# Kernel optimization log

Hardware: AMD Instinct MI355X
Metric: run time of the kernel (lower is better)

Reference implementation:

```python
import jax, jax.numpy as jnp
import numpy as np

EPS = 1e-12  # torch F.normalize eps

def _l2norm(v, axis):
    return v / jnp.maximum(jnp.linalg.norm(v, axis=axis, keepdims=True), EPS)

def setup_inputs() -> dict:
    key = jax.random.key(0)
    k1, k2, k3, k4 = jax.random.split(key, 4)
    n, K, d, H, W = 32, 64, 256, 64, 64
    x = jax.random.normal(k1, (n, d, H, W), dtype=jnp.float32)
    conv_w = jax.random.normal(k2, (K, d), dtype=jnp.float32) * 0.05
    conv_b = jax.random.normal(k3, (K,), dtype=jnp.float32) * 0.05
    centroids = jax.random.uniform(k4, (K, d), dtype=jnp.float32)
    return {"x": x, "conv_w": conv_w, "conv_b": conv_b, "centroids": centroids}

def reference(x, conv_w, conv_b, centroids):
    n, c, H, W = x.shape
    K = centroids.shape[0]
    # input L2 normalization over channel dim
    x = _l2norm(x, axis=1)
    x_flat = x.reshape(n, c, H * W)                      # [n, c, S]
    # 1x1 conv == matmul over channels, then softmax over clusters
    logits = jnp.einsum('kc,ncs->nks', conv_w, x_flat) + conv_b[None, :, None]
    a = jax.nn.softmax(logits, axis=1)                   # [n, K, S]
    # vlad[n,k,c] = sum_s a[n,k,s] * (x[n,c,s] - cent[k,c])
    #            = (a @ x^T) - cent * sum_s a   (GEMM reformulation)
    vlad = jnp.einsum('nks,ncs->nkc', a, x_flat)
    vlad = vlad - a.sum(axis=2)[:, :, None] * centroids[None, :, :]
    # intra-normalize per cluster, flatten, global L2 normalize
    vlad = _l2norm(vlad, axis=2)
    vlad = vlad.reshape(n, K * c)
    vlad = _l2norm(vlad, axis=1)
    return vlad
```

## Files before the change

### kernel.cpp

```cpp
#include <hip/hip_runtime.h>
#include <math.h>

#define NIMG 32
#define CDIM 256
#define KCL  64
#define SPIX 4096

__global__ __launch_bounds__(256) void k_wt(const float* __restrict__ w, float* __restrict__ wT) {
    int g = blockIdx.x * 256 + threadIdx.x;
    if (g < KCL * CDIM) {
        int k = g / CDIM, c = g % CDIM;
        wT[c * KCL + k] = w[g];
    }
}

#define WFMA32() \
    acc[0]=fmaf(w0_.x,xv,acc[0]);   acc[1]=fmaf(w0_.y,xv,acc[1]); \
    acc[2]=fmaf(w0_.z,xv,acc[2]);   acc[3]=fmaf(w0_.w,xv,acc[3]); \
    acc[4]=fmaf(w1_.x,xv,acc[4]);   acc[5]=fmaf(w1_.y,xv,acc[5]); \
    acc[6]=fmaf(w1_.z,xv,acc[6]);   acc[7]=fmaf(w1_.w,xv,acc[7]); \
    acc[8]=fmaf(w2_.x,xv,acc[8]);   acc[9]=fmaf(w2_.y,xv,acc[9]); \
    acc[10]=fmaf(w2_.z,xv,acc[10]); acc[11]=fmaf(w2_.w,xv,acc[11]); \
    acc[12]=fmaf(w3_.x,xv,acc[12]); acc[13]=fmaf(w3_.y,xv,acc[13]); \
    acc[14]=fmaf(w3_.z,xv,acc[14]); acc[15]=fmaf(w3_.w,xv,acc[15]); \
    acc[16]=fmaf(w4_.x,xv,acc[16]); acc[17]=fmaf(w4_.y,xv,acc[17]); \
    acc[18]=fmaf(w4_.z,xv,acc[18]); acc[19]=fmaf(w4_.w,xv,acc[19]); \
    acc[20]=fmaf(w5_.x,xv,acc[20]); acc[21]=fmaf(w5_.y,xv,acc[21]); \
    acc[22]=fmaf(w5_.z,xv,acc[22]); acc[23]=fmaf(w5_.w,xv,acc[23]); \
    acc[24]=fmaf(w6_.x,xv,acc[24]); acc[25]=fmaf(w6_.y,xv,acc[25]); \
    acc[26]=fmaf(w6_.z,xv,acc[26]); acc[27]=fmaf(w6_.w,xv,acc[27]); \
    acc[28]=fmaf(w7_.x,xv,acc[28]); acc[29]=fmaf(w7_.y,xv,acc[29]); \
    acc[30]=fmaf(w7_.z,xv,acc[30]); acc[31]=fmaf(w7_.w,xv,acc[31]);

__global__ __launch_bounds__(512, 4) void k_logits(const float* __restrict__ x,
                                                   const float* __restrict__ wT,
                                                   const float* __restrict__ b,
                                                   float* __restrict__ aT,
                                                   float* __restrict__ inv_norm,
                                                   float* __restrict__ asum_part) {
    int blk = blockIdx.x;
    int n = blk >> 4, g = blk & 15;
    int s0 = g * 256;
    int tid = threadIdx.x;
    int wv = tid >> 6, l = tid & 63;
    int sl = tid & 255;
    int khu = __builtin_amdgcn_readfirstlane(tid >> 8);

    __shared__ float xs[32 * 256];
    __shared__ float4 red4[8 * 64];
    __shared__ float redf[512];
    __shared__ float invs[256];

    float acc[32];
    #pragma unroll
    for (int i = 0; i < 32; i++) acc[i] = 0.f;
    float4 sq = {0.f, 0.f, 0.f, 0.f};

    int cst = tid >> 6;
    int p4 = (tid & 63) * 4;

    for (int t = 0; t < 8; t++) {
        if (t) __syncthreads();
        #pragma unroll
        for (int i = 0; i < 4; i++) {
            int c = cst + 8 * i;
            float4 xq = *(const float4*)(x + ((size_t)(n * CDIM + t * 32 + c)) * SPIX + s0 + p4);
            sq.x = fmaf(xq.x, xq.x, sq.x);
            sq.y = fmaf(xq.y, xq.y, sq.y);
            sq.z = fmaf(xq.z, xq.z, sq.z);
            sq.w = fmaf(xq.w, xq.w, sq.w);
            *(float4*)(xs + c * 256 + p4) = xq;
        }
        __syncthreads();
        const float* wrow = wT + (size_t)(t * 32) * KCL + khu * 32;
        for (int cc = 0; cc < 32; cc++) {
            float xv = xs[cc * 256 + sl];
            const float4* wp = (const float4*)(wrow + (size_t)cc * KCL);
            float4 w0_=wp[0], w1_=wp[1], w2_=wp[2], w3_=wp[3];
            float4 w4_=wp[4], w5_=wp[5], w6_=wp[6], w7_=wp[7];
            WFMA32()
        }
    }

    red4[wv * 64 + l] = sq;
    __syncthreads();
    if (wv == 0) {
        float4 ssq = red4[l];
        #pragma unroll
        for (int i = 1; i < 8; i++) {
            float4 t4 = red4[i * 64 + l];
            ssq.x += t4.x; ssq.y += t4.y; ssq.z += t4.z; ssq.w += t4.w;
        }
        float4 invn;
        invn.x = 1.f / fmaxf(sqrtf(ssq.x), 1e-12f);
        invn.y = 1.f / fmaxf(sqrtf(ssq.y), 1e-12f);
        invn.z = 1.f / fmaxf(sqrtf(ssq.z), 1e-12f);
        invn.w = 1.f / fmaxf(sqrtf(ssq.w), 1e-12f);
        *(float4*)(invs + 4 * l) = invn;
        *(float4*)(inv_norm + (size_t)n * SPIX + s0 + 4 * l) = invn;
    }
    __syncthreads();
    float invp = invs[sl];

    const float* bb = b + khu * 32;
    #pragma unroll
    for (int i = 0; i < 32; i++) acc[i] = fmaf(acc[i], invp, bb[i]);

    float m = acc[0];
    #pragma unroll
    for (int i = 1; i < 32; i++) m = fmaxf(m, acc[i]);
    redf[tid] = m;
    __syncthreads();
    m = fmaxf(redf[sl], redf[256 + sl]);
    float ssum = 0.f;
    #pragma unroll
    for (int i = 0; i < 32; i++) { float e = __expf(acc[i] - m); acc[i] = e; ssum += e; }
    __syncthreads();
    redf[tid] = ssum;
    __syncthreads();
    float r = 1.0f / (redf[sl] + redf[256 + sl]);
    #pragma unroll
    for (int i = 0; i < 32; i++) acc[i] *= r;

    float4* ap = (float4*)(aT + ((size_t)(n * SPIX + s0 + sl)) * KCL + khu * 32);
    #pragma unroll
    for (int j = 0; j < 8; j++) {
        float4 v = {acc[4*j+0], acc[4*j+1], acc[4*j+2], acc[4*j+3]};
        ap[j] = v;
    }

    #pragma unroll
    for (int i = 0; i < 32; i++) {
        float v = acc[i];
        #pragma unroll
        for (int off = 32; off > 0; off >>= 1) v += __shfl_xor(v, off, 64);
        if (l == 0) asum_part[(blk * 8 + wv) * 32 + i] = v;
    }
}

__global__ __launch_bounds__(512, 4) void k_vlad(const float* __restrict__ x,
                                                 const float* __restrict__ inv_norm,
                                                 const float* __restrict__ aT,
                                                 float* __restrict__ vlad_part) {
    int blk = blockIdx.x;
    int n = blk >> 4, g = blk & 15;
    int tid = threadIdx.x;
    int kh = __builtin_amdgcn_readfirstlane(tid >> 8);
    int c = tid & 255;

    __shared__ float xt[256 * 33];

    float acc[32];
    #pragma unroll
    for (int i = 0; i < 32; i++) acc[i] = 0.f;

    int sl = tid & 31;
    int cr = tid >> 5;

    for (int t = 0; t < 8; t++) {
        int s0 = g * 256 + t * 32;
        float invp = inv_norm[n * SPIX + s0 + sl];
        __syncthreads();
        #pragma unroll
        for (int i = 0; i < 16; i++) {
            int cc = cr + i * 16;
            xt[cc * 33 + sl] = x[((size_t)n * CDIM + cc) * SPIX + s0 + sl] * invp;
        }
        __syncthreads();

        const float* ab = aT + ((size_t)(n * SPIX + s0)) * KCL + kh * 32;
        for (int ss = 0; ss < 32; ss++) {
            float xn = xt[c * 33 + ss];
            const float4* ap = (const float4*)(ab + ss * 64);
            #pragma unroll
            for (int q = 0; q < 8; q++) {
                float4 a4 = ap[q];
                acc[4*q+0] = fmaf(a4.x, xn, acc[4*q+0]);
                acc[4*q+1] = fmaf(a4.y, xn, acc[4*q+1]);
                acc[4*q+2] = fmaf(a4.z, xn, acc[4*q+2]);
                acc[4*q+3] = fmaf(a4.w, xn, acc[4*q+3]);
            }
        }
    }
    float* vp = vlad_part + ((size_t)blk * KCL + kh * 32) * CDIM + c;
    #pragma unroll
    for (int i = 0; i < 32; i++) vp[(size_t)i * CDIM] = acc[i];
}

__global__ __launch_bounds__(256) void k_combine(const float* __restrict__ vlad_part,
                                                 const float* __restrict__ asum_part,
                                                 const float* __restrict__ cent,
                                                 float* __restrict__ out,
                                                 float* __restrict__ rs) {
    int blk = blockIdx.x;
    int n = blk >> 6, k = blk & 63;
    int c = threadIdx.x;
    float v = 0.f;
    for (int j = 0; j < 16; j++)
        v += vlad_part[(((size_t)(n * 16 + j)) * KCL + k) * CDIM + c];
    float as = 0.f;
    int kh = k >> 5, kj = k & 31;
    for (int j = 0; j < 16; j++)
        for (int q = 0; q < 4; q++)
            as += asum_part[(((n * 16 + j) * 8) + kh * 4 + q) * 32 + kj];
    v = fmaf(-as, cent[k * CDIM + c], v);

    float t = v * v;
    #pragma unroll
    for (int off = 32; off > 0; off >>= 1) t += __shfl_xor(t, off, 64);
    __shared__ float w4[4];
    int lane = threadIdx.x & 63, wid = threadIdx.x >> 6;
    if (lane == 0) w4[wid] = t;
    __syncthreads();
    float ss = w4[0] + w4[1] + w4[2] + w4[3];
    float inv = 1.0f / fmaxf(sqrtf(ss), 1e-12f);
    out[(size_t)blk * CDIM + c] = v * inv;
    if (threadIdx.x == 0) rs[blk] = ss * inv * inv;
}

__global__ __launch_bounds__(256) void k_gnorm(const float* __restrict__ rs,
                                               float* __restrict__ out) {
    int n = blockIdx.x >> 3, j = blockIdx.x & 7;
    float ss = 0.f;
    for (int k = 0; k < KCL; k++) ss += rs[n * KCL + k];
    float g = 1.0f / fmaxf(sqrtf(ss), 1e-12f);
    size_t base = (size_t)n * (KCL * CDIM) + j * 2048 + threadIdx.x;
    for (int i = 0; i < 8; i++) out[base + i * 256] *= g;
}

extern "C" void kernel_launch(void* const* d_in, const int* in_sizes, int n_in,
                              void* d_out, int out_size, void* d_ws, size_t ws_size,
                              hipStream_t stream) {
    const float* x    = (const float*)d_in[0];
    const float* w    = (const float*)d_in[1];
    const float* b    = (const float*)d_in[2];
    const float* cent = (const float*)d_in[3];
    float* out = (float*)d_out;

    float* ws = (float*)d_ws;
    float* wT        = ws;
    float* inv_norm  = wT + 16384;
    float* aT        = inv_norm + 131072;
    float* vlad_part = aT + 8388608;
    float* asum_part = vlad_part + 8388608;
    float* rs        = asum_part + 131072;

    k_wt<<<64, 256, 0, stream>>>(w, wT);
    k_logits<<<512, 512, 0, stream>>>(x, wT, b, aT, inv_norm, asum_part);
    k_vlad<<<512, 512, 0, stream>>>(x, inv_norm, aT, vlad_part);
    k_combine<<<2048, 256, 0, stream>>>(vlad_part, asum_part, cent, out, rs);
    k_gnorm<<<256, 256, 0, stream>>>(rs, out);
}
```

Before: 184.8 us.

## Double-buffer x tiles via direct global-to-LDS loads and compute norms from LDS

Replaces the register-staged load of each 32-channel x tile with async global_load_lds into a double-buffered shared array, so the next tile is prefetched while the current one is consumed by the FMA loop. The per-pixel squared norm is now accumulated from the LDS values inside the compute loop, which removes the separate cross-wave reduction and its extra shared buffers and barriers. The cost is twice the xs shared memory (64KB), which may reduce occupancy under the 512x4 launch bounds, plus an extra barrier per iteration. It also relies on manual vmcnt waits being correct.

```diff
diff --git a/kernel.cpp b/kernel.cpp
--- a/kernel.cpp
+++ b/kernel.cpp
@@ -45,62 +45,54 @@
     int wv = tid >> 6, l = tid & 63;
     int sl = tid & 255;
     int khu = __builtin_amdgcn_readfirstlane(tid >> 8);
-
-    __shared__ float xs[32 * 256];
-    __shared__ float4 red4[8 * 64];
+    int wvu = __builtin_amdgcn_readfirstlane(wv);
+
+    __shared__ float xs[2][32 * 256];
     __shared__ float redf[512];
-    __shared__ float invs[256];
 
     float acc[32];
     #pragma unroll
     for (int i = 0; i < 32; i++) acc[i] = 0.f;
-    float4 sq = {0.f, 0.f, 0.f, 0.f};
-
-    int cst = tid >> 6;
-    int p4 = (tid & 63) * 4;
+    float nrm = 0.f;
+
+    #define STAGE(T, BUF) { \
+        _Pragma("unroll") \
+        for (int i_ = 0; i_ < 4; i_++) { \
+            int row_ = wvu + 8 * i_; \
+            const float* src_ = x + ((size_t)(n * CDIM + (T) * 32 + row_)) * SPIX + s0 + 4 * l; \
+            float* dst_ = &xs[BUF][row_ * 256] + 4 * l; \
+            __builtin_amdgcn_global_load_lds( \
+                (const __attribute__((address_space(1))) unsigned int*)src_, \
+                (__attribute__((address_space(3))) unsigned int*)dst_, 16, 0, 0); \
+        } }
+
+    STAGE(0, 0)
 
     for (int t = 0; t < 8; t++) {
-        if (t) __syncthreads();
-        #pragma unroll
-        for (int i = 0; i < 4; i++) {
-            int c = cst + 8 * i;
-            float4 xq = *(const float4*)(x + ((size_t)(n * CDIM + t * 32 + c)) * SPIX + s0 + p4);
-            sq.x = fmaf(xq.x, xq.x, sq.x);
-            sq.y = fmaf(xq.y, xq.y, sq.y);
-            sq.z = fmaf(xq.z, xq.z, sq.z);
-            sq.w = fmaf(xq.w, xq.w, sq.w);
-            *(float4*)(xs + c * 256 + p4) = xq;
-        }
-        __syncthreads();
+        int buf = t & 1;
+        if (t < 7) {
+            STAGE(t + 1, buf ^ 1)
+            asm volatile("s_waitcnt vmcnt(4)" ::: "memory");
+        } else {
+            asm volatile("s_waitcnt vmcnt(0)" ::: "memory");
+        }
+        __syncthreads();
+
         const float* wrow = wT + (size_t)(t * 32) * KCL + khu * 32;
+        const float* xrow = xs[buf];
         for (int cc = 0; cc < 32; cc++) {
-            float xv = xs[cc * 256 + sl];
+            float xv = xrow[cc * 256 + sl];
+            nrm = fmaf(xv, xv, nrm);
             const float4* wp = (const float4*)(wrow + (size_t)cc * KCL);
             float4 w0_=wp[0], w1_=wp[1], w2_=wp[2], w3_=wp[3];
             float4 w4_=wp[4], w5_=wp[5], w6_=wp[6], w7_=wp[7];
             WFMA32()
         }
-    }
-
-    red4[wv * 64 + l] = sq;
-    __syncthreads();
-    if (wv == 0) {
-        float4 ssq = red4[l];
-        #pragma unroll
-        for (int i = 1; i < 8; i++) {
-            float4 t4 = red4[i * 64 + l];
-            ssq.x += t4.x; ssq.y += t4.y; ssq.z += t4.z; ssq.w += t4.w;
-        }
-        float4 invn;
-        invn.x = 1.f / fmaxf(sqrtf(ssq.x), 1e-12f);
-        invn.y = 1.f / fmaxf(sqrtf(ssq.y), 1e-12f);
-        invn.z = 1.f / fmaxf(sqrtf(ssq.z), 1e-12f);
-        invn.w = 1.f / fmaxf(sqrtf(ssq.w), 1e-12f);
-        *(float4*)(invs + 4 * l) = invn;
-        *(float4*)(inv_norm + (size_t)n * SPIX + s0 + 4 * l) = invn;
-    }
-    __syncthreads();
-    float invp = invs[sl];
+        __syncthreads();
+    }
+
+    float invp = 1.f / fmaxf(sqrtf(nrm), 1e-12f);
+    if (khu == 0) inv_norm[(size_t)n * SPIX + s0 + sl] = invp;
 
     const float* bb = b + khu * 32;
     #pragma unroll
```

New measurement: 208.8 us. +13.0%, slower.

## Store soft-assignments in k-quad planar layout and move cluster sums to separate kernel

Applied to the files above, without the earlier changes.

The assignment matrix is now written in a planar layout grouped by four clusters per plane, instead of [pixel][64] rows. This lets the k_vlad loads and a new k_asum reduction kernel read contiguous float4 streams. The per-pixel squared norm is now computed from the shared-memory tile inside the channel loop, which removes the cross-wave reduction and two barriers. The shuffle-based asum reduction leaves k_logits and becomes an extra kernel launch that rereads the whole assignment buffer (about 32MB). In k_vlad the 8 float4 loads per pixel now hit 8 separate planes instead of one contiguous 128-byte row.

```diff
diff --git a/kernel.cpp b/kernel.cpp
--- a/kernel.cpp
+++ b/kernel.cpp
@@ -36,25 +36,21 @@
                                                    const float* __restrict__ wT,
                                                    const float* __restrict__ b,
                                                    float* __restrict__ aT,
-                                                   float* __restrict__ inv_norm,
-                                                   float* __restrict__ asum_part) {
+                                                   float* __restrict__ inv_norm) {
     int blk = blockIdx.x;
     int n = blk >> 4, g = blk & 15;
     int s0 = g * 256;
     int tid = threadIdx.x;
-    int wv = tid >> 6, l = tid & 63;
     int sl = tid & 255;
     int khu = __builtin_amdgcn_readfirstlane(tid >> 8);
 
     __shared__ float xs[32 * 256];
-    __shared__ float4 red4[8 * 64];
     __shared__ float redf[512];
-    __shared__ float invs[256];
 
     float acc[32];
     #pragma unroll
     for (int i = 0; i < 32; i++) acc[i] = 0.f;
-    float4 sq = {0.f, 0.f, 0.f, 0.f};
+    float nrm = 0.f;
 
     int cst = tid >> 6;
     int p4 = (tid & 63) * 4;
@@ -65,16 +61,13 @@
         for (int i = 0; i < 4; i++) {
             int c = cst + 8 * i;
             float4 xq = *(const float4*)(x + ((size_t)(n * CDIM + t * 32 + c)) * SPIX + s0 + p4);
-            sq.x = fmaf(xq.x, xq.x, sq.x);
-            sq.y = fmaf(xq.y, xq.y, sq.y);
-            sq.z = fmaf(xq.z, xq.z, sq.z);
-            sq.w = fmaf(xq.w, xq.w, sq.w);
             *(float4*)(xs + c * 256 + p4) = xq;
         }
         __syncthreads();
         const float* wrow = wT + (size_t)(t * 32) * KCL + khu * 32;
         for (int cc = 0; cc < 32; cc++) {
             float xv = xs[cc * 256 + sl];
+            nrm = fmaf(xv, xv, nrm);
             const float4* wp = (const float4*)(wrow + (size_t)cc * KCL);
             float4 w0_=wp[0], w1_=wp[1], w2_=wp[2], w3_=wp[3];
             float4 w4_=wp[4], w5_=wp[5], w6_=wp[6], w7_=wp[7];
@@ -82,25 +75,8 @@
         }
     }
 
-    red4[wv * 64 + l] = sq;
-    __syncthreads();
-    if (wv == 0) {
-        float4 ssq = red4[l];
-        #pragma unroll
-        for (int i = 1; i < 8; i++) {
-            float4 t4 = red4[i * 64 + l];
-            ssq.x += t4.x; ssq.y += t4.y; ssq.z += t4.z; ssq.w += t4.w;
-        }
-        float4 invn;
-        invn.x = 1.f / fmaxf(sqrtf(ssq.x), 1e-12f);
-        invn.y = 1.f / fmaxf(sqrtf(ssq.y), 1e-12f);
-        invn.z = 1.f / fmaxf(sqrtf(ssq.z), 1e-12f);
-        invn.w = 1.f / fmaxf(sqrtf(ssq.w), 1e-12f);
-        *(float4*)(invs + 4 * l) = invn;
-        *(float4*)(inv_norm + (size_t)n * SPIX + s0 + 4 * l) = invn;
-    }
-    __syncthreads();
-    float invp = invs[sl];
+    float invp = 1.f / fmaxf(sqrtf(nrm), 1e-12f);
+    if (khu == 0) inv_norm[(size_t)n * SPIX + s0 + sl] = invp;
 
     const float* bb = b + khu * 32;
     #pragma unroll
@@ -122,19 +98,42 @@
     #pragma unroll
     for (int i = 0; i < 32; i++) acc[i] *= r;
 
-    float4* ap = (float4*)(aT + ((size_t)(n * SPIX + s0 + sl)) * KCL + khu * 32);
+    float* outp = aT + ((size_t)((n * 2 + khu) * 8) * SPIX + s0 + sl) * 4;
     #pragma unroll
     for (int j = 0; j < 8; j++) {
         float4 v = {acc[4*j+0], acc[4*j+1], acc[4*j+2], acc[4*j+3]};
-        ap[j] = v;
-    }
-
-    #pragma unroll
-    for (int i = 0; i < 32; i++) {
-        float v = acc[i];
+        *(float4*)(outp + (size_t)j * SPIX * 4) = v;
+    }
+}
+
+__global__ __launch_bounds__(256) void k_asum(const float* __restrict__ aT,
+                                              float* __restrict__ asum) {
+    int plane = blockIdx.x;
+    int tid = threadIdx.x;
+    const float4* p = (const float4*)(aT + (size_t)plane * SPIX * 4);
+    float4 s = {0.f, 0.f, 0.f, 0.f};
+    for (int i = tid; i < SPIX; i += 256) {
+        float4 v = p[i];
+        s.x += v.x; s.y += v.y; s.z += v.z; s.w += v.w;
+    }
+    __shared__ float4 red[256];
+    red[tid] = s;
+    __syncthreads();
+    if (tid < 64) {
+        float4 a = red[tid], b2 = red[tid + 64], c = red[tid + 128], d = red[tid + 192];
+        a.x += b2.x + c.x + d.x; a.y += b2.y + c.y + d.y;
+        a.z += b2.z + c.z + d.z; a.w += b2.w + c.w + d.w;
         #pragma unroll
-        for (int off = 32; off > 0; off >>= 1) v += __shfl_xor(v, off, 64);
-        if (l == 0) asum_part[(blk * 8 + wv) * 32 + i] = v;
+        for (int off = 32; off > 0; off >>= 1) {
+            a.x += __shfl_xor(a.x, off, 64);
+            a.y += __shfl_xor(a.y, off, 64);
+            a.z += __shfl_xor(a.z, off, 64);
+            a.w += __shfl_xor(a.w, off, 64);
+        }
+        if (tid == 0) {
+            int n = plane >> 4, kh = (plane >> 3) & 1, j = plane & 7;
+            *(float4*)(asum + n * KCL + kh * 32 + j * 4) = a;
+        }
     }
 }
 
@@ -157,6 +156,8 @@
     int sl = tid & 31;
     int cr = tid >> 5;
 
+    const float* abase = aT + (size_t)((n * 2 + kh) * 8) * SPIX * 4;
+
     for (int t = 0; t < 8; t++) {
         int s0 = g * 256 + t * 32;
         float invp = inv_norm[n * SPIX + s0 + sl];
@@ -168,13 +169,12 @@
         }
         __syncthreads();
 
-        const float* ab = aT + ((size_t)(n * SPIX + s0)) * KCL + kh * 32;
         for (int ss = 0; ss < 32; ss++) {
             float xn = xt[c * 33 + ss];
-            const float4* ap = (const float4*)(ab + ss * 64);
+            const float* ap = abase + (size_t)(s0 + ss) * 4;
             #pragma unroll
             for (int q = 0; q < 8; q++) {
-                float4 a4 = ap[q];
+                float4 a4 = *(const float4*)(ap + (size_t)q * SPIX * 4);
                 acc[4*q+0] = fmaf(a4.x, xn, acc[4*q+0]);
                 acc[4*q+1] = fmaf(a4.y, xn, acc[4*q+1]);
                 acc[4*q+2] = fmaf(a4.z, xn, acc[4*q+2]);
@@ -188,7 +188,7 @@
 }
 
 __global__ __launch_bounds__(256) void k_combine(const float* __restrict__ vlad_part,
-                                                 const float* __restrict__ asum_part,
+                                                 const float* __restrict__ asum,
                                                  const float* __restrict__ cent,
                                                  float* __restrict__ out,
                                                  float* __restrict__ rs) {
@@ -198,11 +198,7 @@
     float v = 0.f;
     for (int j = 0; j < 16; j++)
         v += vlad_part[(((size_t)(n * 16 + j)) * KCL + k) * CDIM + c];
-    float as = 0.f;
-    int kh = k >> 5, kj = k & 31;
-    for (int j = 0; j < 16; j++)
-        for (int q = 0; q < 4; q++)
-            as += asum_part[(((n * 16 + j) * 8) + kh * 4 + q) * 32 + kj];
+    float as = asum[n * KCL + k];
     v = fmaf(-as, cent[k * CDIM + c], v);
 
     float t = v * v;
@@ -242,12 +238,13 @@
     float* inv_norm  = wT + 16384;
     float* aT        = inv_norm + 131072;
     float* vlad_part = aT + 8388608;
-    float* asum_part = vlad_part + 8388608;
-    float* rs        = asum_part + 131072;
+    float* asum      = vlad_part + 8388608;
+    float* rs        = asum + 2048;
 
     k_wt<<<64, 256, 0, stream>>>(w, wT);
-    k_logits<<<512, 512, 0, stream>>>(x, wT, b, aT, inv_norm, asum_part);
+    k_logits<<<512, 512, 0, stream>>>(x, wT, b, aT, inv_norm);
+    k_asum<<<512, 256, 0, stream>>>(aT, asum);
     k_vlad<<<512, 512, 0, stream>>>(x, inv_norm, aT, vlad_part);
-    k_combine<<<2048, 256, 0, stream>>>(vlad_part, asum_part, cent, out, rs);
+    k_combine<<<2048, 256, 0, stream>>>(vlad_part, asum, cent, out, rs);
     k_gnorm<<<256, 256, 0, stream>>>(rs, out);
 }
```

Measured after the change: 223.8 us. +21.1%, slower.
